# Performance work log

Measured on AMD Instinct MI355X. Metric: run time of the kernel, lower is better.

The kernel has to match this reference:

```python
import jax, jax.numpy as jnp
import numpy as np
from jax import lax

B, CIN, H, W = 32, 256, 56, 56
COUT, M, K = 256, 2, 3
CMID = COUT * M  # 512
SPARSITY = 0.9


def _make_binary_weight(key):
    k1, k2 = jax.random.split(key)
    shape = (CMID, CIN, K, K)
    mask = jax.random.bernoulli(k1, SPARSITY, shape)
    sign = jax.random.bernoulli(k2, 0.5, shape).astype(jnp.float32) * 2.0 - 1.0
    return jnp.where(mask, sign, 0.0).astype(jnp.float32)


def setup_inputs() -> dict:
    key = jax.random.key(0)
    kx, kw, kfw, kfb = jax.random.split(key, 4)
    x = jax.random.normal(kx, (B, CIN, H, W), dtype=jnp.float32)
    binary_w = _make_binary_weight(kw)
    fan_in = CMID  # 1x1 conv fan-in
    bound = 1.0 / np.sqrt(fan_in)
    fc_w = jax.random.uniform(kfw, (COUT, CMID, 1, 1), minval=-bound, maxval=bound, dtype=jnp.float32)
    fc_b = jax.random.uniform(kfb, (COUT,), minval=-bound, maxval=bound, dtype=jnp.float32)
    return {"x": x, "binary_w": binary_w, "fc_w": fc_w, "fc_b": fc_b}


def reference(x, binary_w, fc_w, fc_b):
    pad = K // 2
    # fixed random ternary conv, stride 1, same padding
    y = lax.conv_general_dilated(
        x, binary_w, window_strides=(1, 1), padding=[(pad, pad), (pad, pad)],
        dimension_numbers=("NCHW", "OIHW", "NCHW"))
    y = jax.nn.relu(y)
    # learnable 1x1 conv with bias
    y = lax.conv_general_dilated(
        y, fc_w, window_strides=(1, 1), padding=[(0, 0), (0, 0)],
        dimension_numbers=("NCHW", "OIHW", "NCHW"))
    return y + fc_b[None, :, None, None]
```

## Files before the change

### kernel.cpp

```cpp
#include <hip/hip_runtime.h>
#include <hip/hip_bf16.h>
#include <stdint.h>


typedef __attribute__((ext_vector_type(8))) short short8;
typedef __attribute__((ext_vector_type(4))) float floatx4;

#define ROWE 8192
#define NT_PER_B 28

#define OFF_WP  0
#define OFF_A2  2359296
#define OFF_XP  2621440
#define OFF_Y   63439872

__device__ static inline void async16(const void* gptr, void* lptr) {
  __builtin_amdgcn_global_load_lds(
      (const __attribute__((address_space(1))) void*)gptr,
      (__attribute__((address_space(3))) void*)lptr,
      16, 0, 0);
}

__device__ static inline unsigned short f2bf(float x) {
  __hip_bfloat16 h = __float2bfloat16(x);
  return *reinterpret_cast<unsigned short*>(&h);
}

__global__ void k_xprep(const float* __restrict__ x, __hip_bfloat16* __restrict__ Xp) {
  const int t = blockIdx.x * 256 + threadIdx.x;
  const int wq  = t & 63;
  const int khi = (t >> 6) & 15;
  const int t2  = t >> 10;
  const int hp  = t2 % 58;
  const int bc  = t2 / 58;
  const int b   = bc >> 1;
  const int cin0 = ((bc & 1) << 7) + (khi << 3);
  const int h = hp - 1, w = wq - 1;
  unsigned short v[8];
  if ((unsigned)h < 56u && (unsigned)w < 56u) {
    const float* xp = x + ((size_t)(b * 256 + cin0) * 56 + h) * 56 + w;
#pragma unroll
    for (int j = 0; j < 8; ++j) v[j] = f2bf(xp[(size_t)j * 3136]);
  } else {
#pragma unroll
    for (int j = 0; j < 8; ++j) v[j] = 0;
  }
  uint4 pk;
  pk.x = (unsigned)v[0] | ((unsigned)v[1] << 16);
  pk.y = (unsigned)v[2] | ((unsigned)v[3] << 16);
  pk.z = (unsigned)v[4] | ((unsigned)v[5] << 16);
  pk.w = (unsigned)v[6] | ((unsigned)v[7] << 16);
  *(uint4*)(Xp + (size_t)t * 8) = pk;
}

__global__ void k_wprep(const float* __restrict__ bw, __hip_bfloat16* __restrict__ Wp) {
  const int idx = blockIdx.x * 256 + threadIdx.x;
  const int klo = idx & 7;
  const int cml = (idx >> 3) & 63;
  const int khi = (idx >> 9) & 15;
  const int cmh = (idx >> 13) & 1;
  const int rest = idx >> 14;
  const int cmblk = rest & 3;
  const int tcg = rest >> 2;
  const int cg  = tcg & 1;
  const int tap = tcg >> 1;
  const int kh = tap / 3, kw = tap - kh * 3;
  const int cm  = (cmblk << 7) + (cmh << 6) + cml;
  const int cin = (cg << 7) + (khi << 3) + klo;
  Wp[idx] = __float2bfloat16(bw[((cm * 256 + cin) * 3 + kh) * 3 + kw]);
}

__global__ void k_a2prep(const float* __restrict__ fw, __hip_bfloat16* __restrict__ A2) {
  const int idx = blockIdx.x * 256 + threadIdx.x;
  const int klo = idx & 7;
  const int cl  = (idx >> 3) & 63;
  const int khi = (idx >> 9) & 15;
  const int ch  = (idx >> 13) & 1;
  const int rest = idx >> 14;
  const int mtile = rest & 1;
  const int cg = rest >> 1;
  const int cout = (mtile << 7) + (ch << 6) + cl;
  const int cm   = (cg << 7) + (khi << 3) + klo;
  A2[idx] = __float2bfloat16(fw[cout * 512 + cm]);
}


#define SB0 __builtin_amdgcn_sched_barrier(0)
#define BARRIER do { SB0; __builtin_amdgcn_s_barrier(); SB0; } while (0)
#define MM(A, B, C) __builtin_amdgcn_mfma_f32_16x16x32_bf16((A), (B), (C), 0, 0, 0)
#define LD8(P) (*(const short8*)(P))

#define MFMA16(MIH, NIH) do { \
  __builtin_amdgcn_s_setprio(1); \
  acc[(MIH)*4+0][(NIH)*2+0] = MM(a0, b0, acc[(MIH)*4+0][(NIH)*2+0]); \
  acc[(MIH)*4+1][(NIH)*2+0] = MM(a1, b0, acc[(MIH)*4+1][(NIH)*2+0]); \
  acc[(MIH)*4+2][(NIH)*2+0] = MM(a2, b0, acc[(MIH)*4+2][(NIH)*2+0]); \
  acc[(MIH)*4+3][(NIH)*2+0] = MM(a3, b0, acc[(MIH)*4+3][(NIH)*2+0]); \
  acc[(MIH)*4+0][(NIH)*2+1] = MM(a0, b1, acc[(MIH)*4+0][(NIH)*2+1]); \
  acc[(MIH)*4+1][(NIH)*2+1] = MM(a1, b1, acc[(MIH)*4+1][(NIH)*2+1]); \
  acc[(MIH)*4+2][(NIH)*2+1] = MM(a2, b1, acc[(MIH)*4+2][(NIH)*2+1]); \
  acc[(MIH)*4+3][(NIH)*2+1] = MM(a3, b1, acc[(MIH)*4+3][(NIH)*2+1]); \
  acc[(MIH)*4+0][(NIH)*2+0] = MM(p0, b2, acc[(MIH)*4+0][(NIH)*2+0]); \
  acc[(MIH)*4+1][(NIH)*2+0] = MM(p1, b2, acc[(MIH)*4+1][(NIH)*2+0]); \
  acc[(MIH)*4+2][(NIH)*2+0] = MM(p2, b2, acc[(MIH)*4+2][(NIH)*2+0]); \
  acc[(MIH)*4+3][(NIH)*2+0] = MM(p3, b2, acc[(MIH)*4+3][(NIH)*2+0]); \
  acc[(MIH)*4+0][(NIH)*2+1] = MM(p0, b3, acc[(MIH)*4+0][(NIH)*2+1]); \
  acc[(MIH)*4+1][(NIH)*2+1] = MM(p1, b3, acc[(MIH)*4+1][(NIH)*2+1]); \
  acc[(MIH)*4+2][(NIH)*2+1] = MM(p2, b3, acc[(MIH)*4+2][(NIH)*2+1]); \
  acc[(MIH)*4+3][(NIH)*2+1] = MM(p3, b3, acc[(MIH)*4+3][(NIH)*2+1]); \
  __builtin_amdgcn_s_setprio(0); \
} while (0)

__global__ __launch_bounds__(512, 2) void k_conv1(
    const __hip_bfloat16* __restrict__ Xp, const __hip_bfloat16* __restrict__ Wp,
    __hip_bfloat16* __restrict__ Y) {
  __shared__ short8 lds_raw[8192];
  char* lds = (char*)lds_raw;
  const int tid  = threadIdx.x;
  const int lane = tid & 63;
  const int wv   = tid >> 6;
  const int wm   = wv >> 2;
  const int wn   = wv & 3;
  const int l15  = lane & 15;
  const int quad = lane >> 4;
  const int id   = blockIdx.x;
  const int xcd  = id & 7;
  const int seq  = id >> 3;
  const int mt   = seq & 1;
  const int nt   = xcd * 56 + (seq >> 1);
  const int b    = nt / 14;
  const int h0   = (nt % 14) * 4;

  const char* WpB = (const char*)Wp;
  const char* XpB = (const char*)Xp;

  const int thrA = ((wv & 3) << 11) + lane * 16;
  const int aRd = wm * 16384 + quad * 1024 + l15 * 16;
  const int bRd = wn * 8192 + quad * 1024 + l15 * 16;

  floatx4 acc[8][4];
#pragma unroll
  for (int i = 0; i < 8; i++)
#pragma unroll
    for (int j = 0; j < 4; j++) acc[i][j] = (floatx4){0.f, 0.f, 0.f, 0.f};

  {
    const char* gA = WpB + (size_t)(2 * mt + wm) * 32768 + thrA;
    const char* gB = XpB + ((size_t)(b * 2) * 58 + h0 + wm) * 16384 + thrA;
    char* sA = lds + wm * 16384 + thrA;
    char* sB = lds + 32768 + wm * 8192 + thrA;
    async16(gA, sA);                     async16(gA + 1024, sA + 1024);
    async16(gB, sB);                     async16(gB + 1024, sB + 1024);
    async16(gB + 32768, sB + 16384);     async16(gB + 32768 + 1024, sB + 16384 + 1024);
    async16(gA + 16384, sA + 8192);      async16(gA + 16384 + 1024, sA + 8192 + 1024);
    asm volatile("s_waitcnt vmcnt(2)" ::: "memory");
    BARRIER;
  }

  auto STEP = [&](int BUF, const char* gA, const char* gB, bool pred) {
    char* ldsC = lds + BUF * 65536;
    char* ldsS = lds + (BUF ^ 1) * 65536;
    const char* Ab = ldsC + aRd;
    const char* Bb = ldsC + 32768 + bRd;
    char* sA = ldsS + wm * 16384 + thrA;
    char* sB = ldsS + 32768 + wm * 8192 + thrA;
    short8 a0, a1, a2, a3, p0, p1, p2, p3, b0, b1, b2, b3;
    a0 = LD8(Ab + 0);     a1 = LD8(Ab + 256);  a2 = LD8(Ab + 512);  a3 = LD8(Ab + 768);
    p0 = LD8(Ab + 4096);  p1 = LD8(Ab + 4352); p2 = LD8(Ab + 4608); p3 = LD8(Ab + 4864);
    b0 = LD8(Bb + 0);     b1 = LD8(Bb + 256);  b2 = LD8(Bb + 4096); b3 = LD8(Bb + 4352);
    if (pred) { async16(gA, sA); async16(gA + 1024, sA + 1024); }
    BARRIER;
    MFMA16(0, 0);
    BARRIER;
    b0 = LD8(Bb + 512);   b1 = LD8(Bb + 768);  b2 = LD8(Bb + 4608); b3 = LD8(Bb + 4864);
    if (pred) { async16(gB, sB); async16(gB + 1024, sB + 1024); }
    BARRIER;
    MFMA16(0, 1);
    if (pred) asm volatile("s_waitcnt vmcnt(4)" ::: "memory");
    else      asm volatile("s_waitcnt vmcnt(0)" ::: "memory");
    BARRIER;
    a0 = LD8(Ab + 8192);  a1 = LD8(Ab + 8448);  a2 = LD8(Ab + 8704);  a3 = LD8(Ab + 8960);
    p0 = LD8(Ab + 12288); p1 = LD8(Ab + 12544); p2 = LD8(Ab + 12800); p3 = LD8(Ab + 13056);
    b0 = LD8(Bb + 0);     b1 = LD8(Bb + 256);   b2 = LD8(Bb + 4096);  b3 = LD8(Bb + 4352);
    if (pred) { async16(gB + 32768, sB + 16384); async16(gB + 32768 + 1024, sB + 16384 + 1024); }
    BARRIER;
    MFMA16(1, 0);
    BARRIER;
    b0 = LD8(Bb + 512);   b1 = LD8(Bb + 768);   b2 = LD8(Bb + 4608);  b3 = LD8(Bb + 4864);
    if (pred) { async16(gA + 16384, sA + 8192); async16(gA + 16384 + 1024, sA + 8192 + 1024); }
    BARRIER;
    MFMA16(1, 1);
    asm volatile("s_waitcnt vmcnt(2)" ::: "memory");
    BARRIER;
  };

  for (int t = 0; t < 18; ++t) {
    const int cg  = t & 1;
    const int tap = t >> 1;
    const int kh = tap / 3, kw = tap - kh * 3;
    const int tn   = t + 1;
    const int cgn  = tn & 1;
    const int tapn = tn >> 1;
    const int khn = tapn / 3, kwn = tapn - khn * 3;
    const char* gA1 = WpB + (size_t)(t * 4 + 2 * mt + wm) * 32768 + 8192 + thrA;
    const char* gB1 = XpB + ((size_t)(b * 2 + cg) * 58 + h0 + kh + wm) * 16384 + kw * 16 + 8192 + thrA;
    const char* gA0 = WpB + (size_t)(tn * 4 + 2 * mt + wm) * 32768 + thrA;
    const char* gB0 = XpB + ((size_t)(b * 2 + cgn) * 58 + h0 + khn + wm) * 16384 + kwn * 16 + thrA;
    STEP(0, gA1, gB1, true);
    STEP(1, gA0, gB0, t < 17);
  }

  const int cmblk = mt * 2 + wm;
  const int ntile = nt * 2 + (wn >> 1);
  const int r2    = wn & 1;
  const size_t ybase = (((size_t)ntile * 4 + cmblk) * 2 + r2) * 8192;
#pragma unroll
  for (int mi = 0; mi < 8; ++mi) {
    const int cml  = mi * 16 + quad * 4;
    const int khi  = cml >> 3;
    const int klo0 = cml & 7;
#pragma unroll
    for (int ni = 0; ni < 4; ++ni) {
      const int w = ni * 16 + l15;
      floatx4 f = acc[mi][ni];
      unsigned lo = (unsigned)f2bf(fmaxf(f[0], 0.f)) | ((unsigned)f2bf(fmaxf(f[1], 0.f)) << 16);
      unsigned hi = (unsigned)f2bf(fmaxf(f[2], 0.f)) | ((unsigned)f2bf(fmaxf(f[3], 0.f)) << 16);
      uint2 pk = make_uint2(lo, hi);
      *(uint2*)((char*)Y + (ybase + (size_t)khi * 512 + w * 8 + klo0) * 2) = pk;
    }
  }
}

__global__ __launch_bounds__(256, 2) void k_conv2(
    const __hip_bfloat16* __restrict__ Y, const __hip_bfloat16* __restrict__ A2,
    const float* __restrict__ fcb, float* __restrict__ out) {
  __shared__ short8 lds_raw[4096];
  char* lds = (char*)lds_raw;
  const int tid  = threadIdx.x;
  const int lane = tid & 63;
  const int wv   = tid >> 6;
  const int wm   = wv >> 1, wn = wv & 1;
  const int l15  = lane & 15;
  const int quad = lane >> 4;
  const int id   = blockIdx.x;
  const int xcd  = id & 7;
  const int seq  = id >> 3;
  const int mtile = seq & 1;
  const int rp    = xcd * 112 + (seq >> 1);

  floatx4 acc[4][4];
#pragma unroll
  for (int i = 0; i < 4; i++)
#pragma unroll
    for (int j = 0; j < 4; j++) acc[i][j] = (floatx4){0.f, 0.f, 0.f, 0.f};

  for (int cg = 0; cg < 4; ++cg) {
    const size_t a_base = (size_t)(cg * 2 + mtile) * 16384;
    const size_t b_base = (size_t)(rp * 4 + cg) * 16384;
    __syncthreads();
    const char* gA = (const char*)(A2 + a_base) + wv * 8192 + lane * 16;
    const char* gB = (const char*)(Y + b_base) + wv * 8192 + lane * 16;
    char* lA = lds + wv * 8192;
    char* lB = lds + 32768 + wv * 8192;
#pragma unroll
    for (int c = 0; c < 8; ++c) {
      async16(gA + c * 1024, lA + c * 1024);
      async16(gB + c * 1024, lB + c * 1024);
    }
    __syncthreads();
#pragma unroll
    for (int kk = 0; kk < 4; ++kk) {
      short8 af[4], bf[4];
#pragma unroll
      for (int mi = 0; mi < 4; ++mi) {
        const int m = wm * 64 + mi * 16 + l15;
        af[mi] = *(const short8*)(lds + ((m >> 6) * 16 + kk * 4 + quad) * 1024 + (m & 63) * 16);
      }
#pragma unroll
      for (int ni = 0; ni < 4; ++ni) {
        const int n = wn * 64 + ni * 16 + l15;
        bf[ni] = *(const short8*)(lds + 32768 + ((n >> 6) * 16 + kk * 4 + quad) * 1024 + (n & 63) * 16);
      }
#pragma unroll
      for (int mi = 0; mi < 4; ++mi)
#pragma unroll
        for (int ni = 0; ni < 4; ++ni)
          acc[mi][ni] = __builtin_amdgcn_mfma_f32_16x16x32_bf16(af[mi], bf[ni], acc[mi][ni], 0, 0, 0);
    }
  }

  const int b   = rp / NT_PER_B;
  const int nb0 = (rp % NT_PER_B) * 128;
#pragma unroll
  for (int mi = 0; mi < 4; ++mi) {
    const int co = mtile * 128 + wm * 64 + mi * 16 + quad * 4;
#pragma unroll
    for (int ni = 0; ni < 4; ++ni) {
      const int n = wn * 64 + ni * 16 + l15;
      const int w = n & 63;
      if (w < 56) {
        const int nb = nb0 + n;
        const int h  = nb >> 6;
        floatx4 f = acc[mi][ni];
        const size_t base = (size_t)(b * 256 + co) * 3136 + h * 56 + w;
#pragma unroll
        for (int r = 0; r < 4; ++r)
          out[base + (size_t)r * 3136] = f[r] + fcb[co + r];
      }
    }
  }
}

extern "C" void kernel_launch(void* const* d_in, const int* in_sizes, int n_in,
                              void* d_out, int out_size, void* d_ws, size_t ws_size,
                              hipStream_t stream) {
  const float* x  = (const float*)d_in[0];
  const float* bw = (const float*)d_in[1];
  const float* fw = (const float*)d_in[2];
  const float* fb = (const float*)d_in[3];
  float* out = (float*)d_out;
  char* ws = (char*)d_ws;

  __hip_bfloat16* Wp = (__hip_bfloat16*)(ws + OFF_WP);
  __hip_bfloat16* A2 = (__hip_bfloat16*)(ws + OFF_A2);
  __hip_bfloat16* Xp = (__hip_bfloat16*)(ws + OFF_XP);
  __hip_bfloat16* Y  = (__hip_bfloat16*)(ws + OFF_Y);

  k_wprep<<<dim3(4608), dim3(256), 0, stream>>>(bw, Wp);
  k_a2prep<<<dim3(512), dim3(256), 0, stream>>>(fw, A2);
  k_xprep<<<dim3(14848), dim3(256), 0, stream>>>(x, Xp);
  k_conv1<<<dim3(896), dim3(512), 0, stream>>>(Xp, Wp, Y);
  k_conv2<<<dim3(1792), dim3(256), 0, stream>>>(Y, A2, fb, out);
}
```

Baseline: 490.6 us.

## Replace per-quarter barriers with one barrier per K-step and prefetch all loads upfront

Restructures the main GEMM loop of the first conv so each step issues all eight async global-to-LDS loads for the next stage at the start, runs the four MFMA quarters separated only by scheduling barriers, and ends with a single full vmcnt(0) wait plus workgroup barrier. The old schedule used five workgroup barriers per step with loads staggered between MFMA groups. The loop is flattened to 36 single steps that alternate buffers, and the MFMA quarter order is changed to reuse the loaded A fragments. This reduces barrier synchronisation overhead, but the wait at step end exposes any global load latency not hidden by a single step of MFMAs.

Result: no change. 485.4 us (-1.1%).

```diff
diff --git a/kernel.cpp b/kernel.cpp
--- a/kernel.cpp
+++ b/kernel.cpp
@@ -86,11 +86,10 @@
 
 
 #define SB0 __builtin_amdgcn_sched_barrier(0)
-#define BARRIER do { SB0; __builtin_amdgcn_s_barrier(); SB0; } while (0)
 #define MM(A, B, C) __builtin_amdgcn_mfma_f32_16x16x32_bf16((A), (B), (C), 0, 0, 0)
 #define LD8(P) (*(const short8*)(P))
 
-#define MFMA16(MIH, NIH) do { \
+#define MFMAQ(MIH, NIH) do { \
   __builtin_amdgcn_s_setprio(1); \
   acc[(MIH)*4+0][(NIH)*2+0] = MM(a0, b0, acc[(MIH)*4+0][(NIH)*2+0]); \
   acc[(MIH)*4+1][(NIH)*2+0] = MM(a1, b0, acc[(MIH)*4+1][(NIH)*2+0]); \
@@ -149,12 +148,14 @@
     const char* gB = XpB + ((size_t)(b * 2) * 58 + h0 + wm) * 16384 + thrA;
     char* sA = lds + wm * 16384 + thrA;
     char* sB = lds + 32768 + wm * 8192 + thrA;
-    async16(gA, sA);                     async16(gA + 1024, sA + 1024);
-    async16(gB, sB);                     async16(gB + 1024, sB + 1024);
-    async16(gB + 32768, sB + 16384);     async16(gB + 32768 + 1024, sB + 16384 + 1024);
-    async16(gA + 16384, sA + 8192);      async16(gA + 16384 + 1024, sA + 8192 + 1024);
-    asm volatile("s_waitcnt vmcnt(2)" ::: "memory");
-    BARRIER;
+    async16(gA, sA);                 async16(gA + 1024, sA + 1024);
+    async16(gB, sB);                 async16(gB + 1024, sB + 1024);
+    async16(gB + 32768, sB + 16384); async16(gB + 32768 + 1024, sB + 16384 + 1024);
+    async16(gA + 16384, sA + 8192);  async16(gA + 16384 + 1024, sA + 8192 + 1024);
+    SB0;
+    asm volatile("s_waitcnt vmcnt(0)" ::: "memory");
+    __builtin_amdgcn_s_barrier();
+    SB0;
   }
 
   auto STEP = [&](int BUF, const char* gA, const char* gB, bool pred) {
@@ -164,50 +165,45 @@
     const char* Bb = ldsC + 32768 + bRd;
     char* sA = ldsS + wm * 16384 + thrA;
     char* sB = ldsS + 32768 + wm * 8192 + thrA;
+    if (pred) {
+      async16(gA, sA);                 async16(gA + 1024, sA + 1024);
+      async16(gB, sB);                 async16(gB + 1024, sB + 1024);
+      async16(gB + 32768, sB + 16384); async16(gB + 32768 + 1024, sB + 16384 + 1024);
+      async16(gA + 16384, sA + 8192);  async16(gA + 16384 + 1024, sA + 8192 + 1024);
+    }
+    SB0;
     short8 a0, a1, a2, a3, p0, p1, p2, p3, b0, b1, b2, b3;
-    a0 = LD8(Ab + 0);     a1 = LD8(Ab + 256);  a2 = LD8(Ab + 512);  a3 = LD8(Ab + 768);
-    p0 = LD8(Ab + 4096);  p1 = LD8(Ab + 4352); p2 = LD8(Ab + 4608); p3 = LD8(Ab + 4864);
-    b0 = LD8(Bb + 0);     b1 = LD8(Bb + 256);  b2 = LD8(Bb + 4096); b3 = LD8(Bb + 4352);
-    if (pred) { async16(gA, sA); async16(gA + 1024, sA + 1024); }
-    BARRIER;
-    MFMA16(0, 0);
-    BARRIER;
-    b0 = LD8(Bb + 512);   b1 = LD8(Bb + 768);  b2 = LD8(Bb + 4608); b3 = LD8(Bb + 4864);
-    if (pred) { async16(gB, sB); async16(gB + 1024, sB + 1024); }
-    BARRIER;
-    MFMA16(0, 1);
-    if (pred) asm volatile("s_waitcnt vmcnt(4)" ::: "memory");
-    else      asm volatile("s_waitcnt vmcnt(0)" ::: "memory");
-    BARRIER;
+    a0 = LD8(Ab + 0);     a1 = LD8(Ab + 256);   a2 = LD8(Ab + 512);   a3 = LD8(Ab + 768);
+    p0 = LD8(Ab + 4096);  p1 = LD8(Ab + 4352);  p2 = LD8(Ab + 4608);  p3 = LD8(Ab + 4864);
+    b0 = LD8(Bb + 0);     b1 = LD8(Bb + 256);   b2 = LD8(Bb + 4096);  b3 = LD8(Bb + 4352);
+    MFMAQ(0, 0);
+    SB0;
+    b0 = LD8(Bb + 512);   b1 = LD8(Bb + 768);   b2 = LD8(Bb + 4608);  b3 = LD8(Bb + 4864);
+    MFMAQ(0, 1);
+    SB0;
     a0 = LD8(Ab + 8192);  a1 = LD8(Ab + 8448);  a2 = LD8(Ab + 8704);  a3 = LD8(Ab + 8960);
     p0 = LD8(Ab + 12288); p1 = LD8(Ab + 12544); p2 = LD8(Ab + 12800); p3 = LD8(Ab + 13056);
+    MFMAQ(1, 1);
+    SB0;
     b0 = LD8(Bb + 0);     b1 = LD8(Bb + 256);   b2 = LD8(Bb + 4096);  b3 = LD8(Bb + 4352);
-    if (pred) { async16(gB + 32768, sB + 16384); async16(gB + 32768 + 1024, sB + 16384 + 1024); }
-    BARRIER;
-    MFMA16(1, 0);
-    BARRIER;
-    b0 = LD8(Bb + 512);   b1 = LD8(Bb + 768);   b2 = LD8(Bb + 4608);  b3 = LD8(Bb + 4864);
-    if (pred) { async16(gA + 16384, sA + 8192); async16(gA + 16384 + 1024, sA + 8192 + 1024); }
-    BARRIER;
-    MFMA16(1, 1);
-    asm volatile("s_waitcnt vmcnt(2)" ::: "memory");
-    BARRIER;
+    MFMAQ(1, 0);
+    SB0;
+    asm volatile("s_waitcnt vmcnt(0)" ::: "memory");
+    __builtin_amdgcn_s_barrier();
+    SB0;
   };
 
-  for (int t = 0; t < 18; ++t) {
-    const int cg  = t & 1;
-    const int tap = t >> 1;
-    const int kh = tap / 3, kw = tap - kh * 3;
-    const int tn   = t + 1;
+  for (int j = 0; j < 36; ++j) {
+    const int jn   = j + 1;
+    const int tn   = jn >> 1;
+    const int sn   = jn & 1;
     const int cgn  = tn & 1;
     const int tapn = tn >> 1;
     const int khn = tapn / 3, kwn = tapn - khn * 3;
-    const char* gA1 = WpB + (size_t)(t * 4 + 2 * mt + wm) * 32768 + 8192 + thrA;
-    const char* gB1 = XpB + ((size_t)(b * 2 + cg) * 58 + h0 + kh + wm) * 16384 + kw * 16 + 8192 + thrA;
-    const char* gA0 = WpB + (size_t)(tn * 4 + 2 * mt + wm) * 32768 + thrA;
-    const char* gB0 = XpB + ((size_t)(b * 2 + cgn) * 58 + h0 + khn + wm) * 16384 + kwn * 16 + thrA;
-    STEP(0, gA1, gB1, true);
-    STEP(1, gA0, gB0, t < 17);
+    const char* gA = WpB + (size_t)(tn * 4 + 2 * mt + wm) * 32768 + sn * 8192 + thrA;
+    const char* gB = XpB + ((size_t)(b * 2 + cgn) * 58 + h0 + khn + wm) * 16384
+                     + kwn * 16 + sn * 8192 + thrA;
+    STEP(j & 1, gA, gB, j < 35);
   }
 
   const int cmblk = mt * 2 + wm;
```
